# Optimization experiments

Measured on AMD Instinct MI355X. Metric: run time of the kernel, lower is better.

## Reference

```python
import jax, jax.numpy as jnp
import numpy as np

N_QUERIES = 2000
N_DOCS = 128
FEATURE_DIM = 220
HIDDEN = 768
N_IDS = 65536


def setup_inputs() -> dict:
    key = jax.random.key(0)
    k1, k2, k3, k4, k5 = jax.random.split(key, 5)
    qid = jax.random.randint(k1, (N_IDS,), 0, N_QUERIES)
    did = jax.random.randint(k2, (N_IDS,), 0, N_DOCS)
    input_feature_id = jnp.stack([qid, did], axis=1).astype(jnp.int64)
    feature_table = jax.random.normal(k3, (N_QUERIES, N_DOCS, FEATURE_DIM), dtype=jnp.float32) * 10.0
    W = jax.random.normal(k4, (HIDDEN, FEATURE_DIM), dtype=jnp.float32) * (1.0 / np.sqrt(FEATURE_DIM))
    b = jax.random.normal(k5, (HIDDEN,), dtype=jnp.float32) * 0.01
    return {"input_feature_id": input_feature_id, "feature_table": feature_table, "W": W, "b": b}


def reference(input_feature_id, feature_table, W, b):
    # fused gather over (query, doc) ids: [N, FEATURE_DIM]
    feat = feature_table[input_feature_id[:, 0], input_feature_id[:, 1]]
    # log-sign transform: log(|x| + 1) * sign(x)
    feature_batch = jnp.log(jnp.abs(feat) + 1.0) * jnp.sign(feat)
    # Linear + ReLU (torch Linear: x @ W^T + b)
    output_embeds = jax.nn.relu(feature_batch @ W.T + b)
    return (output_embeds, feature_batch)
```

## Files before the change

kernel.cpp:

```cpp
#include <hip/hip_runtime.h>
#include <hip/hip_bf16.h>

#define M_TOTAL 65536
#define NQ      2000
#define ND      128
#define FDIM    220
#define KPAD    224
#define HID     768
#define CHUNKS  56

using bf16_t = __hip_bfloat16;
using bf16x8 = __attribute__((ext_vector_type(8))) short;
using f32x4  = __attribute__((ext_vector_type(4))) float;

struct __align__(8) bf4 { bf16_t a, b, c, d; };

__device__ __forceinline__ float slog(float x) {
  return copysignf(log1pf(fabsf(x)), x);
}

__global__ __launch_bounds__(256) void gather_transform_kernel(
    const int* __restrict__ ids, const float* __restrict__ table,
    float* __restrict__ fb_f32, bf16_t* __restrict__ fbB)
{
  int i   = blockIdx.x * 256 + threadIdx.x;
  int row = i / CHUNKS;
  int c4  = i % CHUNKS;
  if (row >= M_TOTAL) return;

  if (c4 == 55) {
    bf4 z; z.a = __float2bfloat16(0.f); z.b = z.a; z.c = z.a; z.d = z.a;
    *(bf4*)(fbB + (size_t)row * KPAD + FDIM) = z;
    return;
  }

  int qid = ids[2 * row];
  int did = ids[2 * row + 1];
  const float4 x =
      *(const float4*)(table + ((size_t)qid * ND + did) * FDIM + c4 * 4);
  float4 y;
  y.x = slog(x.x); y.y = slog(x.y); y.z = slog(x.z); y.w = slog(x.w);
  *(float4*)(fb_f32 + (size_t)row * FDIM + c4 * 4) = y;

  bf4 h;
  h.a = __float2bfloat16(y.x); h.b = __float2bfloat16(y.y);
  h.c = __float2bfloat16(y.z); h.d = __float2bfloat16(y.w);
  *(bf4*)(fbB + (size_t)row * KPAD + c4 * 4) = h;
}

__global__ __launch_bounds__(256) void convert_w_kernel(
    const float* __restrict__ W, bf16_t* __restrict__ Wb)
{
  int i   = blockIdx.x * 256 + threadIdx.x;
  int row = i / CHUNKS;
  int c4  = i % CHUNKS;
  if (row >= HID) return;

  if (c4 == 55) {
    bf4 z; z.a = __float2bfloat16(0.f); z.b = z.a; z.c = z.a; z.d = z.a;
    *(bf4*)(Wb + (size_t)row * KPAD + FDIM) = z;
    return;
  }
  const float4 x = *(const float4*)(W + (size_t)row * FDIM + c4 * 4);
  bf4 h;
  h.a = __float2bfloat16(x.x); h.b = __float2bfloat16(x.y);
  h.c = __float2bfloat16(x.z); h.d = __float2bfloat16(x.w);
  *(bf4*)(Wb + (size_t)row * KPAD + c4 * 4) = h;
}

__global__ __launch_bounds__(256, 2) void gemm_bias_relu_kernel(
    const bf16_t* __restrict__ A, const bf16_t* __restrict__ B,
    const float* __restrict__ bias, float* __restrict__ out)
{
  __shared__ bf16_t As[128 * 32];
  __shared__ bf16_t Bs[128 * 32];

  const int tid  = threadIdx.x;
  const int wave = tid >> 6;
  const int lane = tid & 63;
  const int bn   = blockIdx.x;
  const int bm   = blockIdx.y;
  const int wm   = wave & 1;
  const int wn   = wave >> 1;
  const int l15  = lane & 15;
  const int q    = lane >> 4;

  f32x4 acc[4][4];
#pragma unroll
  for (int i = 0; i < 4; ++i)
#pragma unroll
    for (int j = 0; j < 4; ++j) acc[i][j] = (f32x4){0.f, 0.f, 0.f, 0.f};

  const size_t arow0 = (size_t)bm * 128;
  const size_t brow0 = (size_t)bn * 128;

  for (int k0 = 0; k0 < KPAD; k0 += 32) {
#pragma unroll
    for (int j = 0; j < 2; ++j) {
      const int chbase = j * 256 + wave * 64;
      const int ch     = chbase + lane;
      const int r      = ch >> 2;
      const int cc     = (ch & 3) * 8;
      __builtin_amdgcn_global_load_lds(
          (const __attribute__((address_space(1))) void*)(A + (arow0 + r) * KPAD + k0 + cc),
          (__attribute__((address_space(3))) void*)(As + chbase * 8), 16, 0, 0);
      __builtin_amdgcn_global_load_lds(
          (const __attribute__((address_space(1))) void*)(B + (brow0 + r) * KPAD + k0 + cc),
          (__attribute__((address_space(3))) void*)(Bs + chbase * 8), 16, 0, 0);
    }
    __syncthreads();

    bf16x8 af[4], bg[4];
#pragma unroll
    for (int mi = 0; mi < 4; ++mi)
      af[mi] = *(const bf16x8*)(As + (wm * 64 + mi * 16 + l15) * 32 + q * 8);
#pragma unroll
    for (int ni = 0; ni < 4; ++ni)
      bg[ni] = *(const bf16x8*)(Bs + (wn * 64 + ni * 16 + l15) * 32 + q * 8);

#pragma unroll
    for (int mi = 0; mi < 4; ++mi)
#pragma unroll
      for (int ni = 0; ni < 4; ++ni)
        acc[mi][ni] = __builtin_amdgcn_mfma_f32_16x16x32_bf16(
            af[mi], bg[ni], acc[mi][ni], 0, 0, 0);

    __syncthreads();
  }

  const int col0 = bn * 128 + wn * 64 + l15;
  const int row0 = bm * 128 + wm * 64 + q * 4;
#pragma unroll
  for (int ni = 0; ni < 4; ++ni) {
    const int n    = col0 + ni * 16;
    const float bv = bias[n];
#pragma unroll
    for (int mi = 0; mi < 4; ++mi) {
#pragma unroll
      for (int r = 0; r < 4; ++r) {
        float v = acc[mi][ni][r] + bv;
        out[(size_t)(row0 + mi * 16 + r) * HID + n] = v > 0.f ? v : 0.f;
      }
    }
  }
}

extern "C" void kernel_launch(void* const* d_in, const int* in_sizes, int n_in,
                              void* d_out, int out_size, void* d_ws, size_t ws_size,
                              hipStream_t stream) {
  (void)in_sizes; (void)n_in; (void)out_size; (void)ws_size;

  const int*   ids   = (const int*)d_in[0];
  const float* table = (const float*)d_in[1];
  const float* W     = (const float*)d_in[2];
  const float* bias  = (const float*)d_in[3];

  float* out_embeds = (float*)d_out;
  float* fb_f32     = (float*)d_out + (size_t)M_TOTAL * HID;

  bf16_t* fbB = (bf16_t*)d_ws;
  bf16_t* Wb  = fbB + (size_t)M_TOTAL * KPAD;

  gather_transform_kernel<<<(M_TOTAL * CHUNKS) / 256, 256, 0, stream>>>(
      ids, table, fb_f32, fbB);
  convert_w_kernel<<<(HID * CHUNKS) / 256, 256, 0, stream>>>(W, Wb);

  dim3 grid(HID / 128, M_TOTAL / 128);
  gemm_bias_relu_kernel<<<grid, 256, 0, stream>>>(fbB, Wb, bias, out_embeds);
}
```

Before: 438.0 us.

## Fuse W conversion into GEMM, stage full-K B tile in LDS, read A directly

Drops the separate weight-conversion kernel: each GEMM block now converts its 128-row slice of W from fp32 to bf16 and keeps the whole K extent in padded shared memory. A fragments are loaded straight from global memory into registers, which removes the per-k-step LDS staging and the barriers inside the K loop. Every block now repeats the W conversion, 512 times per weight slice. The padded LDS layout (stride 232) is meant to cut bank conflicts, but the larger tile (about 58KB) may lower occupancy.

```diff
diff --git a/kernel.cpp b/kernel.cpp
--- a/kernel.cpp
+++ b/kernel.cpp
@@ -2,18 +2,19 @@
 #include <hip/hip_bf16.h>
 
 #define M_TOTAL 65536
-#define NQ      2000
 #define ND      128
 #define FDIM    220
 #define KPAD    224
 #define HID     768
 #define CHUNKS  56
+#define BSTRIDE 232
 
 using bf16_t = __hip_bfloat16;
 using bf16x8 = __attribute__((ext_vector_type(8))) short;
 using f32x4  = __attribute__((ext_vector_type(4))) float;
 
-struct __align__(8) bf4 { bf16_t a, b, c, d; };
+struct __align__(8)  bf4    { bf16_t a, b, c, d; };
+struct __align__(16) bf16v8 { bf16_t v[8]; };
 
 __device__ __forceinline__ float slog(float x) {
   return copysignf(log1pf(fabsf(x)), x);
@@ -48,38 +49,40 @@
   *(bf4*)(fbB + (size_t)row * KPAD + c4 * 4) = h;
 }
 
-__global__ __launch_bounds__(256) void convert_w_kernel(
-    const float* __restrict__ W, bf16_t* __restrict__ Wb)
-{
-  int i   = blockIdx.x * 256 + threadIdx.x;
-  int row = i / CHUNKS;
-  int c4  = i % CHUNKS;
-  if (row >= HID) return;
-
-  if (c4 == 55) {
-    bf4 z; z.a = __float2bfloat16(0.f); z.b = z.a; z.c = z.a; z.d = z.a;
-    *(bf4*)(Wb + (size_t)row * KPAD + FDIM) = z;
-    return;
-  }
-  const float4 x = *(const float4*)(W + (size_t)row * FDIM + c4 * 4);
-  bf4 h;
-  h.a = __float2bfloat16(x.x); h.b = __float2bfloat16(x.y);
-  h.c = __float2bfloat16(x.z); h.d = __float2bfloat16(x.w);
-  *(bf4*)(Wb + (size_t)row * KPAD + c4 * 4) = h;
-}
-
 __global__ __launch_bounds__(256, 2) void gemm_bias_relu_kernel(
-    const bf16_t* __restrict__ A, const bf16_t* __restrict__ B,
+    const bf16_t* __restrict__ A, const float* __restrict__ W,
     const float* __restrict__ bias, float* __restrict__ out)
 {
-  __shared__ bf16_t As[128 * 32];
-  __shared__ bf16_t Bs[128 * 32];
+  __shared__ bf16_t Bs[128 * BSTRIDE];
 
-  const int tid  = threadIdx.x;
+  const int tid = threadIdx.x;
+  const int bn  = blockIdx.x;
+  const int bm  = blockIdx.y;
+
+#pragma unroll
+  for (int it = 0; it < 14; ++it) {
+    const int j   = it * 256 + tid;
+    const int row = j / 28;
+    const int g   = j % 28;
+    const float* src = W + (size_t)(bn * 128 + row) * FDIM + g * 8;
+    const float4 f0 = *(const float4*)src;
+    float4 f1;
+    if (g < 27) {
+      f1 = *(const float4*)(src + 4);
+    } else {
+      f1.x = 0.f; f1.y = 0.f; f1.z = 0.f; f1.w = 0.f;
+    }
+    bf16v8 h;
+    h.v[0] = __float2bfloat16(f0.x); h.v[1] = __float2bfloat16(f0.y);
+    h.v[2] = __float2bfloat16(f0.z); h.v[3] = __float2bfloat16(f0.w);
+    h.v[4] = __float2bfloat16(f1.x); h.v[5] = __float2bfloat16(f1.y);
+    h.v[6] = __float2bfloat16(f1.z); h.v[7] = __float2bfloat16(f1.w);
+    *(bf16v8*)(Bs + row * BSTRIDE + g * 8) = h;
+  }
+  __syncthreads();
+
   const int wave = tid >> 6;
   const int lane = tid & 63;
-  const int bn   = blockIdx.x;
-  const int bm   = blockIdx.y;
   const int wm   = wave & 1;
   const int wn   = wave >> 1;
   const int l15  = lane & 15;
@@ -91,41 +94,24 @@
 #pragma unroll
     for (int j = 0; j < 4; ++j) acc[i][j] = (f32x4){0.f, 0.f, 0.f, 0.f};
 
-  const size_t arow0 = (size_t)bm * 128;
-  const size_t brow0 = (size_t)bn * 128;
+  const bf16_t* Abase  = A + (size_t)(bm * 128 + wm * 64 + l15) * KPAD + q * 8;
+  const bf16_t* BsBase = Bs + (wn * 64 + l15) * BSTRIDE + q * 8;
 
-  for (int k0 = 0; k0 < KPAD; k0 += 32) {
 #pragma unroll
-    for (int j = 0; j < 2; ++j) {
-      const int chbase = j * 256 + wave * 64;
-      const int ch     = chbase + lane;
-      const int r      = ch >> 2;
-      const int cc     = (ch & 3) * 8;
-      __builtin_amdgcn_global_load_lds(
-          (const __attribute__((address_space(1))) void*)(A + (arow0 + r) * KPAD + k0 + cc),
-          (__attribute__((address_space(3))) void*)(As + chbase * 8), 16, 0, 0);
-      __builtin_amdgcn_global_load_lds(
-          (const __attribute__((address_space(1))) void*)(B + (brow0 + r) * KPAD + k0 + cc),
-          (__attribute__((address_space(3))) void*)(Bs + chbase * 8), 16, 0, 0);
-    }
-    __syncthreads();
-
+  for (int kb = 0; kb < 7; ++kb) {
     bf16x8 af[4], bg[4];
 #pragma unroll
     for (int mi = 0; mi < 4; ++mi)
-      af[mi] = *(const bf16x8*)(As + (wm * 64 + mi * 16 + l15) * 32 + q * 8);
+      af[mi] = *(const bf16x8*)(Abase + (size_t)mi * 16 * KPAD + kb * 32);
 #pragma unroll
     for (int ni = 0; ni < 4; ++ni)
-      bg[ni] = *(const bf16x8*)(Bs + (wn * 64 + ni * 16 + l15) * 32 + q * 8);
-
+      bg[ni] = *(const bf16x8*)(BsBase + ni * 16 * BSTRIDE + kb * 32);
 #pragma unroll
     for (int mi = 0; mi < 4; ++mi)
 #pragma unroll
       for (int ni = 0; ni < 4; ++ni)
         acc[mi][ni] = __builtin_amdgcn_mfma_f32_16x16x32_bf16(
             af[mi], bg[ni], acc[mi][ni], 0, 0, 0);
-
-    __syncthreads();
   }
 
   const int col0 = bn * 128 + wn * 64 + l15;
@@ -159,12 +145,10 @@
   float* fb_f32     = (float*)d_out + (size_t)M_TOTAL * HID;
 
   bf16_t* fbB = (bf16_t*)d_ws;
-  bf16_t* Wb  = fbB + (size_t)M_TOTAL * KPAD;
 
   gather_transform_kernel<<<(M_TOTAL * CHUNKS) / 256, 256, 0, stream>>>(
       ids, table, fb_f32, fbB);
-  convert_w_kernel<<<(HID * CHUNKS) / 256, 256, 0, stream>>>(W, Wb);
 
   dim3 grid(HID / 128, M_TOTAL / 128);
-  gemm_bias_relu_kernel<<<grid, 256, 0, stream>>>(fbB, Wb, bias, out_embeds);
+  gemm_bias_relu_kernel<<<grid, 256, 0, stream>>>(fbB, W, bias, out_embeds);
 }
```

Measured after the change: 438.0 us. About the same (-0.0%).
